# Kernel optimization log

Measured on AMD Instinct MI355X. Metric: run time of the kernel, lower is better.

Reference implementation:

```python
import jax, jax.numpy as jnp
import numpy as np

N_HEAD = 16

def setup_inputs() -> dict:
    key = jax.random.key(0)
    ks = jax.random.split(key, 5)
    B, T, C = 4, 2048, 1024
    x = jax.random.normal(ks[0], (B, T, C), dtype=jnp.float32)
    # Linear params (torch nn.Linear: y = x @ W.T + b), init scaled like default
    s = 1.0 / np.sqrt(C)
    W_attn = jax.random.uniform(ks[1], (3 * C, C), dtype=jnp.float32, minval=-s, maxval=s)
    b_attn = jax.random.uniform(ks[2], (3 * C,), dtype=jnp.float32, minval=-s, maxval=s)
    W_proj = jax.random.uniform(ks[3], (C, C), dtype=jnp.float32, minval=-s, maxval=s)
    b_proj = jax.random.uniform(ks[4], (C,), dtype=jnp.float32, minval=-s, maxval=s)
    return {"x": x, "W_attn": W_attn, "b_attn": b_attn, "W_proj": W_proj, "b_proj": b_proj}

def reference(x, W_attn, b_attn, W_proj, b_proj):
    B, T, C = x.shape
    H = N_HEAD
    D = C // H
    qkv = jnp.einsum('btc,oc->bto', x, W_attn) + b_attn  # [B,T,3C]
    q, k, v = jnp.split(qkv, 3, axis=2)
    # [B,H,T,D]
    q = q.reshape(B, T, H, D).transpose(0, 2, 1, 3)
    k = k.reshape(B, T, H, D).transpose(0, 2, 1, 3)
    v = v.reshape(B, T, H, D).transpose(0, 2, 1, 3)
    att = jnp.einsum('bhtd,bhsd->bhts', q, k) * (1.0 / np.sqrt(D))  # [B,H,T,T]
    causal = jnp.tril(jnp.ones((T, T), dtype=bool))
    att = jnp.where(causal, att, -jnp.inf)
    att = jax.nn.softmax(att, axis=-1)
    y = jnp.einsum('bhts,bhsd->bhtd', att, v)  # [B,H,T,D]
    y = y.transpose(0, 2, 1, 3).reshape(B, T, C)
    return jnp.einsum('btc,oc->bto', y, W_proj) + b_proj
```

## Files before the change

kernel.cpp:

```cpp
#include <hip/hip_runtime.h>
#include <stdint.h>

typedef unsigned short u16;
typedef __attribute__((ext_vector_type(8))) short short8;
typedef __attribute__((ext_vector_type(4))) float float4v;

#define MFMA16(a, b, c) __builtin_amdgcn_mfma_f32_16x16x32_bf16((a), (b), (c), 0, 0, 0)

#define Q_SCALE 0.18033688011112042f

__device__ __forceinline__ int swz(int row, int col) {
  return row * 64 + (col & 7) + ((((col >> 3) ^ row) & 7) << 3);
}

__device__ __forceinline__ u16 f2b(float f) {
  union { float f; unsigned u; } x; x.f = f;
  unsigned r = x.u + 0x7fffu + ((x.u >> 16) & 1u);
  return (u16)(r >> 16);
}

__device__ __forceinline__ void load_lds_16(const void* g, void* l) {
  __builtin_amdgcn_global_load_lds((__attribute__((address_space(1))) void*)g,
                                   (__attribute__((address_space(3))) void*)l,
                                   16, 0, 0);
}

__global__ __launch_bounds__(256) void cvt_bf16(const float* __restrict__ in,
                                                u16* __restrict__ out, int n8) {
  int i = blockIdx.x * 256 + threadIdx.x;
  if (i >= n8) return;
  const float4* p = (const float4*)in + (size_t)i * 2;
  float4 a = p[0], b = p[1];
  uint4 w;
  w.x = (unsigned)f2b(a.x) | ((unsigned)f2b(a.y) << 16);
  w.y = (unsigned)f2b(a.z) | ((unsigned)f2b(a.w) << 16);
  w.z = (unsigned)f2b(b.x) | ((unsigned)f2b(b.y) << 16);
  w.w = (unsigned)f2b(b.z) | ((unsigned)f2b(b.w) << 16);
  *(uint4*)&out[(size_t)i * 8] = w;
}

__global__ __launch_bounds__(256) void transpose_v(const u16* __restrict__ V,
                                                   u16* __restrict__ Vt) {
  __shared__ u16 tile[64][72];
  const int bh = blockIdx.y;
  const int t0 = blockIdx.x * 64;
  const int tid = threadIdx.x;
  const int r = tid >> 3, c = (tid & 7) * 8;
#pragma unroll
  for (int h = 0; h < 2; ++h) {
    uint4 v = *(const uint4*)&V[((size_t)bh * 2048 + t0 + r + h * 32) * 64 + c];
    const u16* p = (const u16*)&v;
#pragma unroll
    for (int j = 0; j < 8; ++j) tile[c + j][r + h * 32] = p[j];
  }
  __syncthreads();
#pragma unroll
  for (int h = 0; h < 2; ++h) {
    uint4 w;
    u16* p = (u16*)&w;
#pragma unroll
    for (int j = 0; j < 8; ++j) p[j] = tile[r + h * 32][c + j];
    *(uint4*)&Vt[((size_t)bh * 64 + r + h * 32) * 2048 + t0 + c] = w;
  }
}

template <bool QKV_OUT>
__global__ __launch_bounds__(256) void gemm_bt(const u16* __restrict__ A,
                                               const u16* __restrict__ B,
                                               const float* __restrict__ bias,
                                               float* __restrict__ Cf,
                                               u16* __restrict__ QKV,
                                               int M, int N, int K) {
  __shared__ __align__(16) u16 As[128 * 64];
  __shared__ __align__(16) u16 Bs[128 * 64];
  const int tid = threadIdx.x;
  const int lane = tid & 63;
  const int wave = tid >> 6;
  const int quad = lane >> 4;
  const int l15 = lane & 15;
  const int bm0 = blockIdx.y * 128;
  const int bn0 = blockIdx.x * 128;
  const int wm = (wave & 1) * 64;
  const int wn = (wave >> 1) * 64;

  float4v acc[4][4];
#pragma unroll
  for (int i = 0; i < 4; ++i)
#pragma unroll
    for (int j = 0; j < 4; ++j) acc[i][j] = (float4v){0.f, 0.f, 0.f, 0.f};

  const int srow = wave * 32 + (lane >> 3);
  const int scol = ((lane & 7) ^ ((lane >> 3) & 7)) * 8;

  for (int k0 = 0; k0 < K; k0 += 64) {
#pragma unroll
    for (int s = 0; s < 4; ++s) {
      const int r = s * 8;
      load_lds_16(&A[(size_t)(bm0 + srow + r) * K + k0 + scol], &As[(wave * 32 + r) * 64]);
      load_lds_16(&B[(size_t)(bn0 + srow + r) * K + k0 + scol], &Bs[(wave * 32 + r) * 64]);
    }
    __builtin_amdgcn_s_waitcnt(0);
    __syncthreads();
#pragma unroll
    for (int ks = 0; ks < 2; ++ks) {
      short8 af[4], bf[4];
#pragma unroll
      for (int t = 0; t < 4; ++t) {
        af[t] = *(const short8*)&As[swz(wm + t * 16 + l15, ks * 32 + quad * 8)];
        bf[t] = *(const short8*)&Bs[swz(wn + t * 16 + l15, ks * 32 + quad * 8)];
      }
#pragma unroll
      for (int mt = 0; mt < 4; ++mt)
#pragma unroll
        for (int nt = 0; nt < 4; ++nt)
          acc[mt][nt] = MFMA16(af[mt], bf[nt], acc[mt][nt]);
    }
    __syncthreads();
  }

#pragma unroll
  for (int mt = 0; mt < 4; ++mt) {
    const int row0 = bm0 + wm + mt * 16 + quad * 4;
#pragma unroll
    for (int nt = 0; nt < 4; ++nt) {
      const int col = bn0 + wn + nt * 16 + l15;
      const float bs = bias[col];
      if constexpr (QKV_OUT) {
        const int which = col >> 10;
        const int rem = col & 1023;
        const int h = rem >> 6;
        const int d = rem & 63;
        const float sc = (which == 0) ? Q_SCALE : 1.0f;
#pragma unroll
        for (int i = 0; i < 4; ++i) {
          const int t = row0 + i;
          const int b = t >> 11;
          const int tt = t & 2047;
          QKV[(size_t)which * 8388608 +
              ((size_t)(b * 16 + h) * 2048 + tt) * 64 + d] = f2b((acc[mt][nt][i] + bs) * sc);
        }
      } else {
#pragma unroll
        for (int i = 0; i < 4; ++i)
          Cf[(size_t)(row0 + i) * N + col] = acc[mt][nt][i] + bs;
      }
    }
  }
}

__global__ __launch_bounds__(256) void attn_kernel(const u16* __restrict__ QKV,
                                                   const u16* __restrict__ Vt_g,
                                                   u16* __restrict__ Y) {
  const int bx = blockIdx.x;
  const int bh = blockIdx.y;
  const int b = bh >> 4, h = bh & 15;
  const int tid = threadIdx.x;
  const int lane = tid & 63;
  const int wave = tid >> 6;
  const int quad = lane >> 4;
  const int l15 = lane & 15;
  const int qt[2] = {bx, 31 - bx};

  const u16* Qg = QKV + (size_t)bh * 2048 * 64;
  const u16* Kg = QKV + 8388608 + (size_t)bh * 2048 * 64;
  const u16* Vg = Vt_g + (size_t)bh * 64 * 2048;

  __shared__ __align__(16) u16 Ks[2][64 * 64];
  __shared__ __align__(16) u16 Vt[2][64 * 64];
  __shared__ __align__(16) u16 Ps[4][16 * 64];

  short8 qf[2][2];
#pragma unroll
  for (int u = 0; u < 2; ++u)
#pragma unroll
    for (int ks = 0; ks < 2; ++ks)
      qf[u][ks] = *(const short8*)&Qg[(size_t)(qt[u] * 64 + wave * 16 + l15) * 64 + ks * 32 + quad * 8];

  float4v o[2][4];
  float rs[2][4];
#pragma unroll
  for (int u = 0; u < 2; ++u)
#pragma unroll
    for (int i = 0; i < 4; ++i) {
      o[u][i] = (float4v){0.f, 0.f, 0.f, 0.f};
      rs[u][i] = 0.f;
    }

  const int r8 = lane >> 3;
  const int c8 = ((lane & 7) ^ r8) * 8;
  auto stage = [&](int st_, int bufi) {
    const int sb = st_ * 64;
#pragma unroll
    for (int p = 0; p < 2; ++p) {
      const int c = wave * 2 + p;
      load_lds_16(&Kg[(size_t)(sb + c * 8 + r8) * 64 + c8], &Ks[bufi][c * 512]);
      load_lds_16(&Vg[(size_t)(c * 8 + r8) * 2048 + sb + c8], &Vt[bufi][c * 512]);
    }
  };

  const int last = qt[1];
  stage(0, 0);
  __builtin_amdgcn_s_waitcnt(0);
  __syncthreads();

  for (int st = 0; st <= last; ++st) {
    const int cur = st & 1;
    if (st < last) stage(st + 1, cur ^ 1);
    const int sbase = st * 64;
    const bool both = (st <= qt[0]);

    float4v s[2][4];
#pragma unroll
    for (int u = 0; u < 2; ++u)
#pragma unroll
      for (int nt = 0; nt < 4; ++nt) s[u][nt] = (float4v){0.f, 0.f, 0.f, 0.f};
#pragma unroll
    for (int ks = 0; ks < 2; ++ks)
#pragma unroll
      for (int nt = 0; nt < 4; ++nt) {
        const short8 kf = *(const short8*)&Ks[cur][swz(nt * 16 + l15, ks * 32 + quad * 8)];
        s[1][nt] = MFMA16(qf[1][ks], kf, s[1][nt]);
        if (both) s[0][nt] = MFMA16(qf[0][ks], kf, s[0][nt]);
      }

#pragma unroll
    for (int u = 0; u < 2; ++u) {
      if (u == 0 && !both) continue;

      if (st == qt[u]) {
        const int qrow = qt[u] * 64 + wave * 16 + quad * 4;
#pragma unroll
        for (int nt = 0; nt < 4; ++nt) {
          const int kc = sbase + nt * 16 + l15;
#pragma unroll
          for (int i = 0; i < 4; ++i)
            if (kc > qrow + i) s[u][nt][i] = -1e30f;
        }
      }

#pragma unroll
      for (int nt = 0; nt < 4; ++nt)
#pragma unroll
        for (int i = 0; i < 4; ++i) {
          const float p = __builtin_amdgcn_exp2f(s[u][nt][i]);
          s[u][nt][i] = p;
          rs[u][i] += p;
        }

#pragma unroll
      for (int nt = 0; nt < 4; ++nt)
#pragma unroll
        for (int i = 0; i < 4; ++i)
          Ps[wave][swz(quad * 4 + i, nt * 16 + l15)] = f2b(s[u][nt][i]);

#pragma unroll
      for (int ks = 0; ks < 2; ++ks) {
        const short8 pf = *(const short8*)&Ps[wave][swz(l15, ks * 32 + quad * 8)];
#pragma unroll
        for (int dt = 0; dt < 4; ++dt) {
          const short8 vf = *(const short8*)&Vt[cur][swz(dt * 16 + l15, ks * 32 + quad * 8)];
          o[u][dt] = MFMA16(pf, vf, o[u][dt]);
        }
      }
    }

    __builtin_amdgcn_s_waitcnt(0);
    __syncthreads();
  }

#pragma unroll
  for (int u = 0; u < 2; ++u) {
    float linv[4];
#pragma unroll
    for (int i = 0; i < 4; ++i) {
      float r = rs[u][i];
      r += __shfl_xor(r, 1, 16);
      r += __shfl_xor(r, 2, 16);
      r += __shfl_xor(r, 4, 16);
      r += __shfl_xor(r, 8, 16);
      linv[i] = 1.0f / r;
    }
#pragma unroll
    for (int dt = 0; dt < 4; ++dt)
#pragma unroll
      for (int i = 0; i < 4; ++i) {
        const float v = o[u][dt][i] * linv[i];
        const int t = qt[u] * 64 + wave * 16 + quad * 4 + i;
        Y[((size_t)b * 2048 + t) * 1024 + h * 64 + dt * 16 + l15] = f2b(v);
      }
  }
}

extern "C" void kernel_launch(void* const* d_in, const int* in_sizes, int n_in,
                              void* d_out, int out_size, void* d_ws, size_t ws_size,
                              hipStream_t stream) {
  const float* x  = (const float*)d_in[0];
  const float* Wa = (const float*)d_in[1];
  const float* ba = (const float*)d_in[2];
  const float* Wp = (const float*)d_in[3];
  const float* bp = (const float*)d_in[4];
  float* out = (float*)d_out;

  u16* xb  = (u16*)d_ws;
  u16* Wab = xb + 8388608;
  u16* Wpb = Wab + 3145728;
  u16* qkv = Wpb + 1048576;
  u16* y   = xb;
  u16* vt  = (u16*)d_out;

  cvt_bf16<<<4096, 256, 0, stream>>>(x, xb, 1048576);
  cvt_bf16<<<1536, 256, 0, stream>>>(Wa, Wab, 393216);
  cvt_bf16<<<512, 256, 0, stream>>>(Wp, Wpb, 131072);

  gemm_bt<true><<<dim3(24, 64), 256, 0, stream>>>(xb, Wab, ba, nullptr, qkv, 8192, 3072, 1024);
  transpose_v<<<dim3(32, 64), 256, 0, stream>>>(qkv + 16777216, vt);
  attn_kernel<<<dim3(16, 64), 256, 0, stream>>>(qkv, vt, y);
  gemm_bt<false><<<dim3(8, 64), 256, 0, stream>>>(y, Wpb, bp, out, nullptr, 8192, 1024, 1024);
}
```

Before: 297.3 us.

## Give each attention block one query tile, pass P via bpermute

Drops the paired causal query-tile scheme (tile bx with 31-bx per block) in favour of one 64-row query tile per block, doubling the grid to 32x64. S is computed transposed (K as the A operand), so each lane holds probabilities along the key dimension. These are packed to bf16 and redistributed with ds_bpermute into the PV MFMA A-operand layout, replacing the LDS round-trip through Ps. It also adds s_setprio around the MFMA sections. The cost is causal load imbalance across blocks, which now depends on the hardware scheduler, in exchange for fewer registers, no P shared memory and more parallelism.

```diff
diff --git a/kernel.cpp b/kernel.cpp
--- a/kernel.cpp
+++ b/kernel.cpp
@@ -17,6 +17,10 @@
   union { float f; unsigned u; } x; x.f = f;
   unsigned r = x.u + 0x7fffu + ((x.u >> 16) & 1u);
   return (u16)(r >> 16);
+}
+
+__device__ __forceinline__ unsigned pack2(float a, float b) {
+  return (unsigned)f2b(a) | ((unsigned)f2b(b) << 16);
 }
 
 __device__ __forceinline__ void load_lds_16(const void* g, void* l) {
@@ -32,10 +36,10 @@
   const float4* p = (const float4*)in + (size_t)i * 2;
   float4 a = p[0], b = p[1];
   uint4 w;
-  w.x = (unsigned)f2b(a.x) | ((unsigned)f2b(a.y) << 16);
-  w.y = (unsigned)f2b(a.z) | ((unsigned)f2b(a.w) << 16);
-  w.z = (unsigned)f2b(b.x) | ((unsigned)f2b(b.y) << 16);
-  w.w = (unsigned)f2b(b.z) | ((unsigned)f2b(b.w) << 16);
+  w.x = pack2(a.x, a.y);
+  w.y = pack2(a.z, a.w);
+  w.z = pack2(b.x, b.y);
+  w.w = pack2(b.z, b.w);
   *(uint4*)&out[(size_t)i * 8] = w;
 }
 
@@ -159,7 +163,6 @@
   const int wave = tid >> 6;
   const int quad = lane >> 4;
   const int l15 = lane & 15;
-  const int qt[2] = {bx, 31 - bx};
 
   const u16* Qg = QKV + (size_t)bh * 2048 * 64;
   const u16* Kg = QKV + 8388608 + (size_t)bh * 2048 * 64;
@@ -167,24 +170,19 @@
 
   __shared__ __align__(16) u16 Ks[2][64 * 64];
   __shared__ __align__(16) u16 Vt[2][64 * 64];
-  __shared__ __align__(16) u16 Ps[4][16 * 64];
-
-  short8 qf[2][2];
-#pragma unroll
-  for (int u = 0; u < 2; ++u)
-#pragma unroll
-    for (int ks = 0; ks < 2; ++ks)
-      qf[u][ks] = *(const short8*)&Qg[(size_t)(qt[u] * 64 + wave * 16 + l15) * 64 + ks * 32 + quad * 8];
-
-  float4v o[2][4];
-  float rs[2][4];
-#pragma unroll
-  for (int u = 0; u < 2; ++u)
-#pragma unroll
-    for (int i = 0; i < 4; ++i) {
-      o[u][i] = (float4v){0.f, 0.f, 0.f, 0.f};
-      rs[u][i] = 0.f;
-    }
+
+  short8 qf[2];
+#pragma unroll
+  for (int ks = 0; ks < 2; ++ks)
+    qf[ks] = *(const short8*)&Qg[(size_t)(bx * 64 + wave * 16 + l15) * 64 + ks * 32 + quad * 8];
+
+  float4v o[4];
+  float rs = 0.f;
+#pragma unroll
+  for (int i = 0; i < 4; ++i) o[i] = (float4v){0.f, 0.f, 0.f, 0.f};
+
+  const int idxA = (l15 + ((quad & 1) << 5)) << 2;
+  const int idxB = idxA + 64;
 
   const int r8 = lane >> 3;
   const int c8 = ((lane & 7) ^ r8) * 8;
@@ -198,97 +196,97 @@
     }
   };
 
-  const int last = qt[1];
   stage(0, 0);
   __builtin_amdgcn_s_waitcnt(0);
   __syncthreads();
 
-  for (int st = 0; st <= last; ++st) {
+  for (int st = 0; st <= bx; ++st) {
     const int cur = st & 1;
-    if (st < last) stage(st + 1, cur ^ 1);
-    const int sbase = st * 64;
-    const bool both = (st <= qt[0]);
-
-    float4v s[2][4];
-#pragma unroll
-    for (int u = 0; u < 2; ++u)
-#pragma unroll
-      for (int nt = 0; nt < 4; ++nt) s[u][nt] = (float4v){0.f, 0.f, 0.f, 0.f};
+    if (st < bx) stage(st + 1, cur ^ 1);
+
+    float4v s[4];
+#pragma unroll
+    for (int nt = 0; nt < 4; ++nt) s[nt] = (float4v){0.f, 0.f, 0.f, 0.f};
+    __builtin_amdgcn_s_setprio(1);
 #pragma unroll
     for (int ks = 0; ks < 2; ++ks)
 #pragma unroll
       for (int nt = 0; nt < 4; ++nt) {
         const short8 kf = *(const short8*)&Ks[cur][swz(nt * 16 + l15, ks * 32 + quad * 8)];
-        s[1][nt] = MFMA16(qf[1][ks], kf, s[1][nt]);
-        if (both) s[0][nt] = MFMA16(qf[0][ks], kf, s[0][nt]);
+        s[nt] = MFMA16(kf, qf[ks], s[nt]);
       }
-
-#pragma unroll
-    for (int u = 0; u < 2; ++u) {
-      if (u == 0 && !both) continue;
-
-      if (st == qt[u]) {
-        const int qrow = qt[u] * 64 + wave * 16 + quad * 4;
-#pragma unroll
-        for (int nt = 0; nt < 4; ++nt) {
-          const int kc = sbase + nt * 16 + l15;
-#pragma unroll
-          for (int i = 0; i < 4; ++i)
-            if (kc > qrow + i) s[u][nt][i] = -1e30f;
-        }
+    __builtin_amdgcn_s_setprio(0);
+
+    if (st == bx) {
+      const int qrow = wave * 16 + l15;
+      const int kb = quad * 4;
+#pragma unroll
+      for (int nt = 0; nt < 4; ++nt)
+#pragma unroll
+        for (int i = 0; i < 4; ++i)
+          if (kb + nt * 16 + i > qrow) s[nt][i] = -1e30f;
+    }
+
+    uint2 pk[4];
+#pragma unroll
+    for (int nt = 0; nt < 4; ++nt) {
+      const float p0 = __builtin_amdgcn_exp2f(s[nt][0]);
+      const float p1 = __builtin_amdgcn_exp2f(s[nt][1]);
+      const float p2 = __builtin_amdgcn_exp2f(s[nt][2]);
+      const float p3 = __builtin_amdgcn_exp2f(s[nt][3]);
+      rs += (p0 + p1) + (p2 + p3);
+      pk[nt].x = pack2(p0, p1);
+      pk[nt].y = pack2(p2, p3);
+    }
+
+    short8 af[2];
+    const bool hi = quad >= 2;
+#pragma unroll
+    for (int ks = 0; ks < 2; ++ks) {
+      const int a0 = __builtin_amdgcn_ds_bpermute(idxA, (int)pk[2 * ks].x);
+      const int a1 = __builtin_amdgcn_ds_bpermute(idxA, (int)pk[2 * ks].y);
+      const int b0 = __builtin_amdgcn_ds_bpermute(idxA, (int)pk[2 * ks + 1].x);
+      const int b1 = __builtin_amdgcn_ds_bpermute(idxA, (int)pk[2 * ks + 1].y);
+      const int c0 = __builtin_amdgcn_ds_bpermute(idxB, (int)pk[2 * ks].x);
+      const int c1 = __builtin_amdgcn_ds_bpermute(idxB, (int)pk[2 * ks].y);
+      const int d0 = __builtin_amdgcn_ds_bpermute(idxB, (int)pk[2 * ks + 1].x);
+      const int d1 = __builtin_amdgcn_ds_bpermute(idxB, (int)pk[2 * ks + 1].y);
+      uint4 w;
+      w.x = (unsigned)(hi ? b0 : a0);
+      w.y = (unsigned)(hi ? b1 : a1);
+      w.z = (unsigned)(hi ? d0 : c0);
+      w.w = (unsigned)(hi ? d1 : c1);
+      af[ks] = *(const short8*)&w;
+    }
+
+    __builtin_amdgcn_s_setprio(1);
+#pragma unroll
+    for (int ks = 0; ks < 2; ++ks)
+#pragma unroll
+      for (int dt = 0; dt < 4; ++dt) {
+        const short8 vf = *(const short8*)&Vt[cur][swz(dt * 16 + l15, ks * 32 + quad * 8)];
+        o[dt] = MFMA16(af[ks], vf, o[dt]);
       }
-
-#pragma unroll
-      for (int nt = 0; nt < 4; ++nt)
-#pragma unroll
-        for (int i = 0; i < 4; ++i) {
-          const float p = __builtin_amdgcn_exp2f(s[u][nt][i]);
-          s[u][nt][i] = p;
-          rs[u][i] += p;
-        }
-
-#pragma unroll
-      for (int nt = 0; nt < 4; ++nt)
-#pragma unroll
-        for (int i = 0; i < 4; ++i)
-          Ps[wave][swz(quad * 4 + i, nt * 16 + l15)] = f2b(s[u][nt][i]);
-
-#pragma unroll
-      for (int ks = 0; ks < 2; ++ks) {
-        const short8 pf = *(const short8*)&Ps[wave][swz(l15, ks * 32 + quad * 8)];
-#pragma unroll
-        for (int dt = 0; dt < 4; ++dt) {
-          const short8 vf = *(const short8*)&Vt[cur][swz(dt * 16 + l15, ks * 32 + quad * 8)];
-          o[u][dt] = MFMA16(pf, vf, o[u][dt]);
-        }
-      }
-    }
+    __builtin_amdgcn_s_setprio(0);
 
     __builtin_amdgcn_s_waitcnt(0);
     __syncthreads();
   }
 
-#pragma unroll
-  for (int u = 0; u < 2; ++u) {
-    float linv[4];
+  float r = rs;
+  r += __shfl_xor(r, 16);
+  r += __shfl_xor(r, 32);
+  float linv[4];
+#pragma unroll
+  for (int i = 0; i < 4; ++i) linv[i] = 1.0f / __shfl(r, quad * 4 + i);
+#pragma unroll
+  for (int dt = 0; dt < 4; ++dt)
 #pragma unroll
     for (int i = 0; i < 4; ++i) {
-      float r = rs[u][i];
-      r += __shfl_xor(r, 1, 16);
-      r += __shfl_xor(r, 2, 16);
-      r += __shfl_xor(r, 4, 16);
-      r += __shfl_xor(r, 8, 16);
-      linv[i] = 1.0f / r;
-    }
-#pragma unroll
-    for (int dt = 0; dt < 4; ++dt)
-#pragma unroll
-      for (int i = 0; i < 4; ++i) {
-        const float v = o[u][dt][i] * linv[i];
-        const int t = qt[u] * 64 + wave * 16 + quad * 4 + i;
-        Y[((size_t)b * 2048 + t) * 1024 + h * 64 + dt * 16 + l15] = f2b(v);
-      }
-  }
+      const float v = o[dt][i] * linv[i];
+      const int t = bx * 64 + wave * 16 + quad * 4 + i;
+      Y[((size_t)b * 2048 + t) * 1024 + h * 64 + dt * 16 + l15] = f2b(v);
+    }
 }
 
 extern "C" void kernel_launch(void* const* d_in, const int* in_sizes, int n_in,
@@ -314,6 +312,6 @@
 
   gemm_bt<true><<<dim3(24, 64), 256, 0, stream>>>(xb, Wab, ba, nullptr, qkv, 8192, 3072, 1024);
   transpose_v<<<dim3(32, 64), 256, 0, stream>>>(qkv + 16777216, vt);
-  attn_kernel<<<dim3(16, 64), 256, 0, stream>>>(qkv, vt, y);
+  attn_kernel<<<dim3(32, 64), 256, 0, stream>>>(qkv, vt, y);
   gemm_bt<false><<<dim3(8, 64), 256, 0, stream>>>(y, Wpb, bp, out, nullptr, 8192, 1024, 1024);
 }
```

After: 320.7 us. +7.9%, slower.
